# Performance work log

Hardware: AMD Instinct MI355X
Metric: run time of the kernel (lower is better)

The kernel has to match this reference:

```python
import jax, jax.numpy as jnp
import numpy as np

D = 256  # out_size / d_model
B, S = 8, 4096


def setup_inputs() -> dict:
    key = jax.random.key(0)
    ks = jax.random.split(key, 10)
    std = 1.0 / np.sqrt(D)
    x = jax.random.normal(ks[0], (B, S, D), dtype=jnp.float32)
    Wq = jax.random.uniform(ks[1], (D, D), jnp.float32, -std, std)
    bq = jax.random.uniform(ks[2], (D,), jnp.float32, -std, std)
    Wk = jax.random.uniform(ks[3], (D, D), jnp.float32, -std, std)
    bk = jax.random.uniform(ks[4], (D,), jnp.float32, -std, std)
    Wv = jax.random.uniform(ks[5], (D, D), jnp.float32, -std, std)
    bv = jax.random.uniform(ks[6], (D,), jnp.float32, -std, std)
    Wo = jax.random.uniform(ks[7], (D, D), jnp.float32, -std, std)
    bo = jax.random.uniform(ks[8], (D,), jnp.float32, -std, std)
    cv = jax.random.normal(ks[9], (D, 1), dtype=jnp.float32)
    return {"x": x, "Wq": Wq, "bq": bq, "Wk": Wk, "bk": bk,
            "Wv": Wv, "bv": bv, "Wo": Wo, "bo": bo, "cv": cv}


def reference(x, Wq, bq, Wk, bk, Wv, bv, Wo, bo, cv):
    # Local single-head attention: separate matmul / softmax / matmul
    q = jnp.einsum('bsd,de->bse', x, Wq) + bq
    k = jnp.einsum('bsd,de->bse', x, Wk) + bk
    v = jnp.einsum('bsd,de->bse', x, Wv) + bv
    scale = jnp.sqrt(jnp.asarray(D, dtype=x.dtype))
    scores = jnp.einsum('bqd,bkd->bqk', q, k) / scale  # [B,S,S]
    attn = jax.nn.softmax(scores, axis=-1)
    ctx = jnp.einsum('bqk,bkd->bqd', attn, v)
    logits = jnp.einsum('bsd,de->bse', ctx, Wo) + bo
    # Global context-vector pooling weights (softmax over sequence dim)
    w = jnp.einsum('bsd,dk->bsk', logits, cv)          # [B,S,1]
    nw = jax.nn.softmax(w, axis=1)
    return logits * nw
```

## Files before the change

### kernel.cpp

```cpp
#include <hip/hip_runtime.h>
#include <math.h>
#include <cstddef>
#include <cstdint>

#define B_ 8
#define S_ 4096
#define D_ 256

typedef __attribute__((ext_vector_type(8))) short short8v;
typedef __attribute__((ext_vector_type(4))) short short4v;
typedef __attribute__((ext_vector_type(4))) float float4v;

__device__ __forceinline__ unsigned short f2bf(float f) {
  unsigned u = __float_as_uint(f);
  return (unsigned short)((u + 0x7FFF + ((u >> 16) & 1)) >> 16);
}
__device__ __forceinline__ float bf2f(unsigned short h) {
  return __uint_as_float((unsigned)h << 16);
}
__device__ __forceinline__ unsigned packp(float p) {
  const unsigned short hh = f2bf(p);
  const unsigned short ll = f2bf(p - bf2f(hh));
  return ((unsigned)hh << 16) | (unsigned)ll;
}

__global__ __launch_bounds__(256) void wsplit_kernel(
    const float* __restrict__ Wq, const float* __restrict__ Wk,
    const float* __restrict__ Wv, const float* __restrict__ Wo,
    short* __restrict__ wsp) {
  const int mat = blockIdx.x >> 4;
  const int k0  = (blockIdx.x & 15) << 4;
  const float* W = (mat == 0) ? Wq : (mat == 1) ? Wk : (mat == 2) ? Wv : Wo;
  const int n = threadIdx.x;
  short8v h0, h1, l0, l1;
#pragma unroll
  for (int j = 0; j < 8; ++j) {
    float y = W[(size_t)(k0 + j) * 256 + n];
    unsigned short hh = f2bf(y);
    h0[j] = (short)hh; l0[j] = (short)f2bf(y - bf2f(hh));
    y = W[(size_t)(k0 + 8 + j) * 256 + n];
    hh = f2bf(y);
    h1[j] = (short)hh; l1[j] = (short)f2bf(y - bf2f(hh));
  }
  short* dh = wsp + (size_t)mat * 131072 + (size_t)n * 256 + k0;
  short* dl = dh + 65536;
  *(short8v*)(dh + 0) = h0; *(short8v*)(dh + 8) = h1;
  *(short8v*)(dl + 0) = l0; *(short8v*)(dl + 8) = l1;
}

__global__ __launch_bounds__(512, 2) void proj_qkv_mfma(
    const float* __restrict__ x, const short* __restrict__ wsp,
    const float* __restrict__ bq, const float* __restrict__ bk,
    const float* __restrict__ bvv,
    short* __restrict__ qh, short* __restrict__ ql,
    short* __restrict__ kh, short* __restrict__ kl,
    short* __restrict__ vth, short* __restrict__ vtl) {
  __shared__ __align__(16) short sWh[256 * 40];
  __shared__ __align__(16) short sWl[256 * 40];

  const int t    = threadIdx.x;
  const int w    = t >> 6;
  const int lane = t & 63;
  const int m    = lane & 15;
  const int quad = lane >> 4;
  const size_t r0 = (size_t)blockIdx.x * 128;
  const size_t srow = r0 + 16 * w + m;

  short8v xh[8], xl[8];
#pragma unroll
  for (int kk = 0; kk < 8; ++kk) {
    const float* xp = x + srow * 256 + kk * 32 + quad * 8;
    const float4 a = *(const float4*)xp;
    const float4 b2 = *(const float4*)(xp + 4);
    const float v[8] = {a.x, a.y, a.z, a.w, b2.x, b2.y, b2.z, b2.w};
    short8v h, l;
#pragma unroll
    for (int e = 0; e < 8; ++e) {
      const unsigned short hh = f2bf(v[e]);
      h[e] = (short)hh; l[e] = (short)f2bf(v[e] - bf2f(hh));
    }
    xh[kk] = h; xl[kk] = l;
  }

  const int nr   = t >> 1;
  const int kh16 = (t & 1) << 4;
  short8v rh0, rh1, rl0, rl1;
  {
    const short* gh = wsp + (size_t)nr * 256 + kh16;
    const short* gl = gh + 65536;
    rh0 = *(const short8v*)gh;       rh1 = *(const short8v*)(gh + 8);
    rl0 = *(const short8v*)gl;       rl1 = *(const short8v*)(gl + 8);
  }

#pragma unroll
  for (int p = 0; p < 3; ++p) {
    float4v acc[16];
#pragma unroll
    for (int nt = 0; nt < 16; ++nt) acc[nt] = (float4v){0.f, 0.f, 0.f, 0.f};

    for (int kk = 0; kk < 8; ++kk) {
      asm volatile("s_waitcnt lgkmcnt(0)" ::: "memory");
      __builtin_amdgcn_s_barrier();
      asm volatile("" ::: "memory");
      *(short8v*)&sWh[nr * 40 + kh16]     = rh0;
      *(short8v*)&sWh[nr * 40 + kh16 + 8] = rh1;
      *(short8v*)&sWl[nr * 40 + kh16]     = rl0;
      *(short8v*)&sWl[nr * 40 + kh16 + 8] = rl1;
      {
        const int np = (kk < 7) ? p : p + 1;
        const int nk = (kk < 7) ? kk + 1 : 0;
        if (np < 3) {
          const short* gh = wsp + (size_t)np * 131072 +
                            (size_t)nr * 256 + nk * 32 + kh16;
          const short* gl = gh + 65536;
          rh0 = *(const short8v*)gh;   rh1 = *(const short8v*)(gh + 8);
          rl0 = *(const short8v*)gl;   rl1 = *(const short8v*)(gl + 8);
        }
      }
      asm volatile("s_waitcnt lgkmcnt(0)" ::: "memory");
      __builtin_amdgcn_s_barrier();
      asm volatile("" ::: "memory");

      __builtin_amdgcn_s_setprio(1);
#pragma unroll
      for (int nt = 0; nt < 16; ++nt) {
        const short8v wh = *(const short8v*)&sWh[(nt * 16 + m) * 40 + quad * 8];
        const short8v wl = *(const short8v*)&sWl[(nt * 16 + m) * 40 + quad * 8];
        if (p < 2) {
          acc[nt] = __builtin_amdgcn_mfma_f32_16x16x32_bf16(wh, xh[kk], acc[nt], 0, 0, 0);
          acc[nt] = __builtin_amdgcn_mfma_f32_16x16x32_bf16(wh, xl[kk], acc[nt], 0, 0, 0);
          acc[nt] = __builtin_amdgcn_mfma_f32_16x16x32_bf16(wl, xh[kk], acc[nt], 0, 0, 0);
        } else {
          acc[nt] = __builtin_amdgcn_mfma_f32_16x16x32_bf16(xh[kk], wh, acc[nt], 0, 0, 0);
          acc[nt] = __builtin_amdgcn_mfma_f32_16x16x32_bf16(xh[kk], wl, acc[nt], 0, 0, 0);
          acc[nt] = __builtin_amdgcn_mfma_f32_16x16x32_bf16(xl[kk], wh, acc[nt], 0, 0, 0);
        }
      }
      __builtin_amdgcn_s_setprio(0);
    }

    if (p < 2) {
      const float scale = (p == 0) ? 0.0625f : 1.0f;
      short* oh = (p == 0) ? qh : kh;
      short* ol = (p == 0) ? ql : kl;
      const float* bias = (p == 0) ? bq : bk;
#pragma unroll
      for (int nt = 0; nt < 16; ++nt) {
        const float4 bb = *(const float4*)(bias + nt * 16 + quad * 4);
        const float bb4[4] = {bb.x, bb.y, bb.z, bb.w};
        short4v h4, l4;
#pragma unroll
        for (int r = 0; r < 4; ++r) {
          const float y = (acc[nt][r] + bb4[r]) * scale;
          const unsigned short hh = f2bf(y);
          h4[r] = (short)hh; l4[r] = (short)f2bf(y - bf2f(hh));
        }
        *(short4v*)(oh + srow * 256 + nt * 16 + quad * 4) = h4;
        *(short4v*)(ol + srow * 256 + nt * 16 + quad * 4) = l4;
      }
    } else {
      const int bidx = (int)(r0 >> 12);
      const size_t bD = (size_t)bidx * (D_ * (size_t)S_);
      const int sl0 = (int)(r0 & 4095) + 16 * w + quad * 4;
#pragma unroll
      for (int nt = 0; nt < 16; ++nt) {
        const int d = nt * 16 + m;
        const float bn = bvv[d];
        short4v h4, l4;
#pragma unroll
        for (int r = 0; r < 4; ++r) {
          const float y = acc[nt][r] + bn;
          const unsigned short hh = f2bf(y);
          h4[r] = (short)hh; l4[r] = (short)f2bf(y - bf2f(hh));
        }
        *(short4v*)(vth + bD + (size_t)d * S_ + sl0) = h4;
        *(short4v*)(vtl + bD + (size_t)d * S_ + sl0) = l4;
      }
    }
  }
}

__global__ __launch_bounds__(512, 2) void gemm_out_mfma(
    const float* __restrict__ ctx, const short* __restrict__ wsp,
    const float* __restrict__ bo, const float* __restrict__ cv,
    float* __restrict__ out, float* __restrict__ wvec) {
  __shared__ __align__(16) short sWh[256 * 40];
  __shared__ __align__(16) short sWl[256 * 40];

  const int t    = threadIdx.x;
  const int w    = t >> 6;
  const int lane = t & 63;
  const int m    = lane & 15;
  const int quad = lane >> 4;
  const size_t r0 = (size_t)blockIdx.x * 128;
  const size_t srow = r0 + 16 * w + m;
  const short* wbase = wsp + (size_t)3 * 131072;

  short8v ah[8], al[8];
#pragma unroll
  for (int kk = 0; kk < 8; ++kk) {
    const float* xp = ctx + srow * 256 + kk * 32 + quad * 8;
    const float4 a = *(const float4*)xp;
    const float4 b2 = *(const float4*)(xp + 4);
    const float v[8] = {a.x, a.y, a.z, a.w, b2.x, b2.y, b2.z, b2.w};
    short8v h, l;
#pragma unroll
    for (int e = 0; e < 8; ++e) {
      const unsigned short hh = f2bf(v[e]);
      h[e] = (short)hh; l[e] = (short)f2bf(v[e] - bf2f(hh));
    }
    ah[kk] = h; al[kk] = l;
  }

  const int nr   = t >> 1;
  const int kh16 = (t & 1) << 4;
  short8v rh0, rh1, rl0, rl1;
  {
    const short* gh = wbase + (size_t)nr * 256 + kh16;
    const short* gl = gh + 65536;
    rh0 = *(const short8v*)gh;       rh1 = *(const short8v*)(gh + 8);
    rl0 = *(const short8v*)gl;       rl1 = *(const short8v*)(gl + 8);
  }

  float4v acc[16];
#pragma unroll
  for (int nt = 0; nt < 16; ++nt) acc[nt] = (float4v){0.f, 0.f, 0.f, 0.f};

  for (int kk = 0; kk < 8; ++kk) {
    asm volatile("s_waitcnt lgkmcnt(0)" ::: "memory");
    __builtin_amdgcn_s_barrier();
    asm volatile("" ::: "memory");
    *(short8v*)&sWh[nr * 40 + kh16]     = rh0;
    *(short8v*)&sWh[nr * 40 + kh16 + 8] = rh1;
    *(short8v*)&sWl[nr * 40 + kh16]     = rl0;
    *(short8v*)&sWl[nr * 40 + kh16 + 8] = rl1;
    if (kk < 7) {
      const short* gh = wbase + (size_t)nr * 256 + (kk + 1) * 32 + kh16;
      const short* gl = gh + 65536;
      rh0 = *(const short8v*)gh;   rh1 = *(const short8v*)(gh + 8);
      rl0 = *(const short8v*)gl;   rl1 = *(const short8v*)(gl + 8);
    }
    asm volatile("s_waitcnt lgkmcnt(0)" ::: "memory");
    __builtin_amdgcn_s_barrier();
    asm volatile("" ::: "memory");

    __builtin_amdgcn_s_setprio(1);
#pragma unroll
    for (int nt = 0; nt < 16; ++nt) {
      const short8v wh = *(const short8v*)&sWh[(nt * 16 + m) * 40 + quad * 8];
      const short8v wl = *(const short8v*)&sWl[(nt * 16 + m) * 40 + quad * 8];
      acc[nt] = __builtin_amdgcn_mfma_f32_16x16x32_bf16(wh, ah[kk], acc[nt], 0, 0, 0);
      acc[nt] = __builtin_amdgcn_mfma_f32_16x16x32_bf16(wh, al[kk], acc[nt], 0, 0, 0);
      acc[nt] = __builtin_amdgcn_mfma_f32_16x16x32_bf16(wl, ah[kk], acc[nt], 0, 0, 0);
    }
    __builtin_amdgcn_s_setprio(0);
  }

  float wp = 0.f;
  float* orow = out + srow * 256;
#pragma unroll
  for (int nt = 0; nt < 16; ++nt) {
    const float4 bb = *(const float4*)(bo + nt * 16 + quad * 4);
    const float4 cc = *(const float4*)(cv + nt * 16 + quad * 4);
    float4 o;
    o.x = acc[nt][0] + bb.x; o.y = acc[nt][1] + bb.y;
    o.z = acc[nt][2] + bb.z; o.w = acc[nt][3] + bb.w;
    wp += o.x * cc.x + o.y * cc.y + o.z * cc.z + o.w * cc.w;
    *(float4*)(orow + nt * 16 + quad * 4) = o;
  }
  wp += __shfl_xor(wp, 16, 64);
  wp += __shfl_xor(wp, 32, 64);
  if (quad == 0) wvec[srow] = wp;
}

__global__ __launch_bounds__(512, 2) void flash_attn_mfma(
    const short* __restrict__ qh, const short* __restrict__ ql,
    const short* __restrict__ kh, const short* __restrict__ kl,
    const short* __restrict__ vth, const short* __restrict__ vtl,
    float* __restrict__ ctx) {
  __shared__ __align__(16) short sK[16896];
  __shared__ __align__(16) short sV[2][20480];
  __shared__ __align__(16) unsigned int sP[2][8][16][36];

  const int t    = threadIdx.x;
  const int w    = t >> 6;
  const int lane = t & 63;
  const int m    = lane & 15;
  const int quad = lane >> 4;
  const int q0   = blockIdx.x * 128;
  const int b    = blockIdx.y;
  const size_t sd = (size_t)b * (S_ * (size_t)D_);
  const size_t bD = (size_t)b * (D_ * (size_t)S_);

  short8v aqh[8], aql[8];
  {
    const size_t row = sd + (size_t)(q0 + 16 * w + m) * D_;
#pragma unroll
    for (int kk = 0; kk < 8; ++kk) {
      const size_t off = row + kk * 32 + quad * 8;
      aqh[kk] = *(const short8v*)(qh + off);
      aql[kk] = *(const short8v*)(ql + off);
    }
  }

  short8v ones;
#pragma unroll
  for (int e = 0; e < 8; ++e) ones[e] = (short)0x3F80;

  float4v acc[16];
#pragma unroll
  for (int dt = 0; dt < 16; ++dt) acc[dt] = (float4v){0.f, 0.f, 0.f, 0.f};
  float4v accl = (float4v){0.f, 0.f, 0.f, 0.f};
  float m_i = -INFINITY;

  const int kr0 = t >> 5;
  const int kc0 = (t & 31) << 3;
  const int vd  = t >> 1;
  const int vjh = (t & 1) << 4;

  short8v rKh0, rKh1, rKl0, rKl1;
  short8v rVh0, rVh1, rVl0, rVl1;

  {
    const size_t g0 = sd + (size_t)kr0 * D_ + kc0;
    const size_t g1 = sd + (size_t)(16 + kr0) * D_ + kc0;
    rKh0 = *(const short8v*)(kh + g0);
    rKh1 = *(const short8v*)(kh + g1);
    rKl0 = *(const short8v*)(kl + g0);
    rKl1 = *(const short8v*)(kl + g1);
  }

  for (int jt = 0; jt < 128; ++jt) {
    const int j0  = jt << 5;
    const int cur = jt & 1;
    const int old = cur ^ 1;

    *(short8v*)&sK[kr0 * 264 + kc0]               = rKh0;
    *(short8v*)&sK[(16 + kr0) * 264 + kc0]        = rKh1;
    *(short8v*)&sK[8448 + kr0 * 264 + kc0]        = rKl0;
    *(short8v*)&sK[8448 + (16 + kr0) * 264 + kc0] = rKl1;
    {
      const size_t g = bD + (size_t)vd * S_ + j0 + vjh;
      rVh0 = *(const short8v*)(vth + g);
      rVh1 = *(const short8v*)(vth + g + 8);
      rVl0 = *(const short8v*)(vtl + g);
      rVl1 = *(const short8v*)(vtl + g + 8);
    }
    asm volatile("s_waitcnt lgkmcnt(0)" ::: "memory");
    __builtin_amdgcn_s_barrier();
    asm volatile("" ::: "memory");

    float4v s0 = (float4v){0.f, 0.f, 0.f, 0.f};
    float4v s1 = (float4v){0.f, 0.f, 0.f, 0.f};
    __builtin_amdgcn_s_setprio(1);
#pragma unroll
    for (int kk = 0; kk < 8; ++kk) {
      const int co = kk * 32 + quad * 8;
      const short8v bh0 = *(const short8v*)&sK[m * 264 + co];
      const short8v bl0 = *(const short8v*)&sK[8448 + m * 264 + co];
      const short8v bh1 = *(const short8v*)&sK[(16 + m) * 264 + co];
      const short8v bl1 = *(const short8v*)&sK[8448 + (16 + m) * 264 + co];
      s0 = __builtin_amdgcn_mfma_f32_16x16x32_bf16(bh0, aqh[kk], s0, 0, 0, 0);
      s0 = __builtin_amdgcn_mfma_f32_16x16x32_bf16(bh0, aql[kk], s0, 0, 0, 0);
      s0 = __builtin_amdgcn_mfma_f32_16x16x32_bf16(bl0, aqh[kk], s0, 0, 0, 0);
      s1 = __builtin_amdgcn_mfma_f32_16x16x32_bf16(bh1, aqh[kk], s1, 0, 0, 0);
      s1 = __builtin_amdgcn_mfma_f32_16x16x32_bf16(bh1, aql[kk], s1, 0, 0, 0);
      s1 = __builtin_amdgcn_mfma_f32_16x16x32_bf16(bl1, aqh[kk], s1, 0, 0, 0);
    }
    __builtin_amdgcn_s_setprio(0);

    float alpha_p = 1.0f;
    bool fired = false;
    {
      float mx = fmaxf(fmaxf(fmaxf(s0[0], s0[1]), fmaxf(s0[2], s0[3])),
                       fmaxf(fmaxf(s1[0], s1[1]), fmaxf(s1[2], s1[3])));
      mx = fmaxf(mx, __shfl_xor(mx, 16, 64));
      mx = fmaxf(mx, __shfl_xor(mx, 32, 64));
      if (__any(mx > m_i + 8.0f)) {
        const float mnew = fmaxf(m_i, mx);
        alpha_p = __expf(m_i - mnew);
        m_i = mnew;
        fired = true;
      }
    }

    {
      uint4 w0, w1;
      w0.x = packp(__expf(s0[0] - m_i));
      w0.y = packp(__expf(s0[1] - m_i));
      w0.z = packp(__expf(s0[2] - m_i));
      w0.w = packp(__expf(s0[3] - m_i));
      w1.x = packp(__expf(s1[0] - m_i));
      w1.y = packp(__expf(s1[1] - m_i));
      w1.z = packp(__expf(s1[2] - m_i));
      w1.w = packp(__expf(s1[3] - m_i));
      *(uint4*)&sP[cur][w][m][4 * quad]      = w0;
      *(uint4*)&sP[cur][w][m][16 + 4 * quad] = w1;
    }

    if (jt > 0) {
      short8v ph, pl;
      {
        const uint4 pa = *(const uint4*)&sP[old][w][m][quad * 8];
        const uint4 pb = *(const uint4*)&sP[old][w][m][quad * 8 + 4];
        ph[0] = (short)(pa.x >> 16); pl[0] = (short)(pa.x & 0xffff);
        ph[1] = (short)(pa.y >> 16); pl[1] = (short)(pa.y & 0xffff);
        ph[2] = (short)(pa.z >> 16); pl[2] = (short)(pa.z & 0xffff);
        ph[3] = (short)(pa.w >> 16); pl[3] = (short)(pa.w & 0xffff);
        ph[4] = (short)(pb.x >> 16); pl[4] = (short)(pb.x & 0xffff);
        ph[5] = (short)(pb.y >> 16); pl[5] = (short)(pb.y & 0xffff);
        ph[6] = (short)(pb.z >> 16); pl[6] = (short)(pb.z & 0xffff);
        ph[7] = (short)(pb.w >> 16); pl[7] = (short)(pb.w & 0xffff);
      }
      const short* sVo = &sV[old][0];
      __builtin_amdgcn_s_setprio(1);
      accl = __builtin_amdgcn_mfma_f32_16x16x32_bf16(ph, ones, accl, 0, 0, 0);
      accl = __builtin_amdgcn_mfma_f32_16x16x32_bf16(pl, ones, accl, 0, 0, 0);
#pragma unroll
      for (int dt = 0; dt < 16; ++dt) {
        const int vr = (dt * 16 + m) * 40 + quad * 8;
        const short8v bh = *(const short8v*)&sVo[vr];
        const short8v bl = *(const short8v*)&sVo[10240 + vr];
        acc[dt] = __builtin_amdgcn_mfma_f32_16x16x32_bf16(ph, bh, acc[dt], 0, 0, 0);
        acc[dt] = __builtin_amdgcn_mfma_f32_16x16x32_bf16(ph, bl, acc[dt], 0, 0, 0);
        acc[dt] = __builtin_amdgcn_mfma_f32_16x16x32_bf16(pl, bh, acc[dt], 0, 0, 0);
      }
      __builtin_amdgcn_s_setprio(0);
    }

    if (fired) {
      float al[4];
#pragma unroll
      for (int r = 0; r < 4; ++r) al[r] = __shfl(alpha_p, 20 * quad + r, 64);
#pragma unroll
      for (int dt = 0; dt < 16; ++dt)
#pragma unroll
        for (int r = 0; r < 4; ++r) acc[dt][r] *= al[r];
#pragma unroll
      for (int r = 0; r < 4; ++r) accl[r] *= al[r];
    }

    {
      short* sVc = &sV[cur][0];
      *(short8v*)&sVc[vd * 40 + vjh]             = rVh0;
      *(short8v*)&sVc[vd * 40 + vjh + 8]         = rVh1;
      *(short8v*)&sVc[10240 + vd * 40 + vjh]     = rVl0;
      *(short8v*)&sVc[10240 + vd * 40 + vjh + 8] = rVl1;
    }
    if (jt < 127) {
      const int j0n = j0 + 32;
      const size_t g0 = sd + (size_t)(j0n + kr0) * D_ + kc0;
      const size_t g1 = sd + (size_t)(j0n + 16 + kr0) * D_ + kc0;
      rKh0 = *(const short8v*)(kh + g0);
      rKh1 = *(const short8v*)(kh + g1);
      rKl0 = *(const short8v*)(kl + g0);
      rKl1 = *(const short8v*)(kl + g1);
    }
    asm volatile("s_waitcnt lgkmcnt(0)" ::: "memory");
    __builtin_amdgcn_s_barrier();
    asm volatile("" ::: "memory");
  }

  {
    short8v ph, pl;
    {
      const uint4 pa = *(const uint4*)&sP[1][w][m][quad * 8];
      const uint4 pb = *(const uint4*)&sP[1][w][m][quad * 8 + 4];
      ph[0] = (short)(pa.x >> 16); pl[0] = (short)(pa.x & 0xffff);
      ph[1] = (short)(pa.y >> 16); pl[1] = (short)(pa.y & 0xffff);
      ph[2] = (short)(pa.z >> 16); pl[2] = (short)(pa.z & 0xffff);
      ph[3] = (short)(pa.w >> 16); pl[3] = (short)(pa.w & 0xffff);
      ph[4] = (short)(pb.x >> 16); pl[4] = (short)(pb.x & 0xffff);
      ph[5] = (short)(pb.y >> 16); pl[5] = (short)(pb.y & 0xffff);
      ph[6] = (short)(pb.z >> 16); pl[6] = (short)(pb.z & 0xffff);
      ph[7] = (short)(pb.w >> 16); pl[7] = (short)(pb.w & 0xffff);
    }
    const short* sVo = &sV[1][0];
    accl = __builtin_amdgcn_mfma_f32_16x16x32_bf16(ph, ones, accl, 0, 0, 0);
    accl = __builtin_amdgcn_mfma_f32_16x16x32_bf16(pl, ones, accl, 0, 0, 0);
#pragma unroll
    for (int dt = 0; dt < 16; ++dt) {
      const int vr = (dt * 16 + m) * 40 + quad * 8;
      const short8v bh = *(const short8v*)&sVo[vr];
      const short8v bl = *(const short8v*)&sVo[10240 + vr];
      acc[dt] = __builtin_amdgcn_mfma_f32_16x16x32_bf16(ph, bh, acc[dt], 0, 0, 0);
      acc[dt] = __builtin_amdgcn_mfma_f32_16x16x32_bf16(ph, bl, acc[dt], 0, 0, 0);
      acc[dt] = __builtin_amdgcn_mfma_f32_16x16x32_bf16(pl, bh, acc[dt], 0, 0, 0);
    }
  }

#pragma unroll
  for (int r = 0; r < 4; ++r) {
    const float inv = 1.0f / accl[r];
    float* cp = ctx + sd + (size_t)(q0 + 16 * w + quad * 4 + r) * D_ + m;
#pragma unroll
    for (int dt = 0; dt < 16; ++dt) cp[dt * 16] = acc[dt][r] * inv;
  }
}

__global__ __launch_bounds__(256) void softmax_scale_kernel(
    float* __restrict__ out, const float* __restrict__ wv) {
  __shared__ float red[4];
  const int t = threadIdx.x;
  const int wave = t >> 6, lane = t & 63;
  const int b = blockIdx.x >> 8;
  const float* wb = wv + (size_t)b * S_;

  float mx = -INFINITY;
#pragma unroll
  for (int i = 0; i < 16; ++i) mx = fmaxf(mx, wb[t + (i << 8)]);
#pragma unroll
  for (int off = 32; off > 0; off >>= 1) mx = fmaxf(mx, __shfl_xor(mx, off, 64));
  if (lane == 0) red[wave] = mx;
  __syncthreads();
  const float M = fmaxf(fmaxf(red[0], red[1]), fmaxf(red[2], red[3]));
  float sum = 0.f;
#pragma unroll
  for (int i = 0; i < 16; ++i) sum += __expf(wb[t + (i << 8)] - M);
#pragma unroll
  for (int off = 32; off > 0; off >>= 1) sum += __shfl_xor(sum, off, 64);
  __syncthreads();
  if (lane == 0) red[wave] = sum;
  __syncthreads();
  const float inv = 1.0f / (red[0] + red[1] + red[2] + red[3]);

  float4* o4 = (float4*)out;
  const size_t g0 = (size_t)blockIdx.x * 1024 + t;
#pragma unroll
  for (int i = 0; i < 4; ++i) {
    const size_t g = g0 + (size_t)(i << 8);
    const float sc = __expf(wv[g >> 6] - M) * inv;
    float4 vv = o4[g];
    vv.x *= sc; vv.y *= sc; vv.z *= sc; vv.w *= sc;
    o4[g] = vv;
  }
}

extern "C" void kernel_launch(void* const* d_in, const int* in_sizes, int n_in,
                              void* d_out, int out_size, void* d_ws, size_t ws_size,
                              hipStream_t stream) {
  const float* x  = (const float*)d_in[0];
  const float* Wq = (const float*)d_in[1];
  const float* bq = (const float*)d_in[2];
  const float* Wk = (const float*)d_in[3];
  const float* bk = (const float*)d_in[4];
  const float* Wv = (const float*)d_in[5];
  const float* bv = (const float*)d_in[6];
  const float* Wo = (const float*)d_in[7];
  const float* bo = (const float*)d_in[8];
  const float* cv = (const float*)d_in[9];
  float* out = (float*)d_out;

  const size_t N = (size_t)B_ * S_ * D_;
  short* qh  = (short*)d_ws;
  short* ql  = qh + N;
  short* kh  = ql + N;
  short* kl  = kh + N;
  short* vth = kl + N;
  short* vtl = vth + N;
  float* ctx = (float*)(vtl + N);
  float* w   = ctx + N;
  short* wsp = (short*)(w + (size_t)B_ * S_);

  wsplit_kernel<<<64, 256, 0, stream>>>(Wq, Wk, Wv, Wo, wsp);
  proj_qkv_mfma<<<256, 512, 0, stream>>>(x, wsp, bq, bk, bv,
                                         qh, ql, kh, kl, vth, vtl);
  flash_attn_mfma<<<dim3(32, 8), 512, 0, stream>>>(qh, ql, kh, kl, vth, vtl, ctx);
  gemm_out_mfma<<<256, 512, 0, stream>>>(ctx, wsp, bo, cv, out, w);
  softmax_scale_kernel<<<2048, 256, 0, stream>>>(out, w);
}
```

Before: 598.5 us.

## Split PV matmul across waves by output column tiles, single-buffer sV/sP

```diff
diff --git a/kernel.cpp b/kernel.cpp
--- a/kernel.cpp
+++ b/kernel.cpp
@@ -279,8 +279,11 @@
     const short* __restrict__ vth, const short* __restrict__ vtl,
     float* __restrict__ ctx) {
   __shared__ __align__(16) short sK[16896];
-  __shared__ __align__(16) short sV[2][20480];
-  __shared__ __align__(16) unsigned int sP[2][8][16][36];
+  __shared__ __align__(16) short sV[20480];
+  __shared__ __align__(16) unsigned int sP[8][16][36];
+  __shared__ __align__(16) float sAlpha[8][16];
+  __shared__ __align__(16) int sF[8];
+  __shared__ __align__(16) float sL[128];
 
   const int t    = threadIdx.x;
   const int w    = t >> 6;
@@ -307,9 +310,12 @@
 #pragma unroll
   for (int e = 0; e < 8; ++e) ones[e] = (short)0x3F80;
 
-  float4v acc[16];
-#pragma unroll
-  for (int dt = 0; dt < 16; ++dt) acc[dt] = (float4v){0.f, 0.f, 0.f, 0.f};
+  float4v acc[8][2];
+#pragma unroll
+  for (int qt = 0; qt < 8; ++qt) {
+    acc[qt][0] = (float4v){0.f, 0.f, 0.f, 0.f};
+    acc[qt][1] = (float4v){0.f, 0.f, 0.f, 0.f};
+  }
   float4v accl = (float4v){0.f, 0.f, 0.f, 0.f};
   float m_i = -INFINITY;
 
@@ -331,9 +337,7 @@
   }
 
   for (int jt = 0; jt < 128; ++jt) {
-    const int j0  = jt << 5;
-    const int cur = jt & 1;
-    const int old = cur ^ 1;
+    const int j0 = jt << 5;
 
     *(short8v*)&sK[kr0 * 264 + kc0]               = rKh0;
     *(short8v*)&sK[(16 + kr0) * 264 + kc0]        = rKh1;
@@ -370,7 +374,7 @@
     __builtin_amdgcn_s_setprio(0);
 
     float alpha_p = 1.0f;
-    bool fired = false;
+    int fired = 0;
     {
       float mx = fmaxf(fmaxf(fmaxf(s0[0], s0[1]), fmaxf(s0[2], s0[3])),
                        fmaxf(fmaxf(s1[0], s1[1]), fmaxf(s1[2], s1[3])));
@@ -380,9 +384,16 @@
         const float mnew = fmaxf(m_i, mx);
         alpha_p = __expf(m_i - mnew);
         m_i = mnew;
-        fired = true;
-      }
-    }
+        fired = 1;
+        float al[4];
+#pragma unroll
+        for (int r = 0; r < 4; ++r) al[r] = __shfl(alpha_p, 20 * quad + r, 64);
+#pragma unroll
+        for (int r = 0; r < 4; ++r) accl[r] *= al[r];
+      }
+    }
+    if (quad == 0) sAlpha[w][m] = alpha_p;
+    if (lane == 0) sF[w] = fired;
 
     {
       uint4 w0, w1;
@@ -394,59 +405,14 @@
       w1.y = packp(__expf(s1[1] - m_i));
       w1.z = packp(__expf(s1[2] - m_i));
       w1.w = packp(__expf(s1[3] - m_i));
-      *(uint4*)&sP[cur][w][m][4 * quad]      = w0;
-      *(uint4*)&sP[cur][w][m][16 + 4 * quad] = w1;
-    }
-
-    if (jt > 0) {
-      short8v ph, pl;
-      {
-        const uint4 pa = *(const uint4*)&sP[old][w][m][quad * 8];
-        const uint4 pb = *(const uint4*)&sP[old][w][m][quad * 8 + 4];
-        ph[0] = (short)(pa.x >> 16); pl[0] = (short)(pa.x & 0xffff);
-        ph[1] = (short)(pa.y >> 16); pl[1] = (short)(pa.y & 0xffff);
-        ph[2] = (short)(pa.z >> 16); pl[2] = (short)(pa.z & 0xffff);
-        ph[3] = (short)(pa.w >> 16); pl[3] = (short)(pa.w & 0xffff);
-        ph[4] = (short)(pb.x >> 16); pl[4] = (short)(pb.x & 0xffff);
-        ph[5] = (short)(pb.y >> 16); pl[5] = (short)(pb.y & 0xffff);
-        ph[6] = (short)(pb.z >> 16); pl[6] = (short)(pb.z & 0xffff);
-        ph[7] = (short)(pb.w >> 16); pl[7] = (short)(pb.w & 0xffff);
-      }
-      const short* sVo = &sV[old][0];
-      __builtin_amdgcn_s_setprio(1);
-      accl = __builtin_amdgcn_mfma_f32_16x16x32_bf16(ph, ones, accl, 0, 0, 0);
-      accl = __builtin_amdgcn_mfma_f32_16x16x32_bf16(pl, ones, accl, 0, 0, 0);
-#pragma unroll
-      for (int dt = 0; dt < 16; ++dt) {
-        const int vr = (dt * 16 + m) * 40 + quad * 8;
-        const short8v bh = *(const short8v*)&sVo[vr];
-        const short8v bl = *(const short8v*)&sVo[10240 + vr];
-        acc[dt] = __builtin_amdgcn_mfma_f32_16x16x32_bf16(ph, bh, acc[dt], 0, 0, 0);
-        acc[dt] = __builtin_amdgcn_mfma_f32_16x16x32_bf16(ph, bl, acc[dt], 0, 0, 0);
-        acc[dt] = __builtin_amdgcn_mfma_f32_16x16x32_bf16(pl, bh, acc[dt], 0, 0, 0);
-      }
-      __builtin_amdgcn_s_setprio(0);
-    }
-
-    if (fired) {
-      float al[4];
-#pragma unroll
-      for (int r = 0; r < 4; ++r) al[r] = __shfl(alpha_p, 20 * quad + r, 64);
-#pragma unroll
-      for (int dt = 0; dt < 16; ++dt)
-#pragma unroll
-        for (int r = 0; r < 4; ++r) acc[dt][r] *= al[r];
-#pragma unroll
-      for (int r = 0; r < 4; ++r) accl[r] *= al[r];
-    }
-
-    {
-      short* sVc = &sV[cur][0];
-      *(short8v*)&sVc[vd * 40 + vjh]             = rVh0;
-      *(short8v*)&sVc[vd * 40 + vjh + 8]         = rVh1;
-      *(short8v*)&sVc[10240 + vd * 40 + vjh]     = rVl0;
-      *(short8v*)&sVc[10240 + vd * 40 + vjh + 8] = rVl1;
-    }
+      *(uint4*)&sP[w][m][4 * quad]      = w0;
+      *(uint4*)&sP[w][m][16 + 4 * quad] = w1;
+    }
+
+    *(short8v*)&sV[vd * 40 + vjh]               = rVh0;
+    *(short8v*)&sV[vd * 40 + vjh + 8]           = rVh1;
+    *(short8v*)&sV[10240 + vd * 40 + vjh]       = rVl0;
+    *(short8v*)&sV[10240 + vd * 40 + vjh + 8]   = rVl1;
     if (jt < 127) {
       const int j0n = j0 + 32;
       const size_t g0 = sd + (size_t)(j0n + kr0) * D_ + kc0;
@@ -459,42 +425,79 @@
     asm volatile("s_waitcnt lgkmcnt(0)" ::: "memory");
     __builtin_amdgcn_s_barrier();
     asm volatile("" ::: "memory");
-  }
-
-  {
-    short8v ph, pl;
+
     {
-      const uint4 pa = *(const uint4*)&sP[1][w][m][quad * 8];
-      const uint4 pb = *(const uint4*)&sP[1][w][m][quad * 8 + 4];
-      ph[0] = (short)(pa.x >> 16); pl[0] = (short)(pa.x & 0xffff);
-      ph[1] = (short)(pa.y >> 16); pl[1] = (short)(pa.y & 0xffff);
-      ph[2] = (short)(pa.z >> 16); pl[2] = (short)(pa.z & 0xffff);
-      ph[3] = (short)(pa.w >> 16); pl[3] = (short)(pa.w & 0xffff);
-      ph[4] = (short)(pb.x >> 16); pl[4] = (short)(pb.x & 0xffff);
-      ph[5] = (short)(pb.y >> 16); pl[5] = (short)(pb.y & 0xffff);
-      ph[6] = (short)(pb.z >> 16); pl[6] = (short)(pb.z & 0xffff);
-      ph[7] = (short)(pb.w >> 16); pl[7] = (short)(pb.w & 0xffff);
-    }
-    const short* sVo = &sV[1][0];
-    accl = __builtin_amdgcn_mfma_f32_16x16x32_bf16(ph, ones, accl, 0, 0, 0);
-    accl = __builtin_amdgcn_mfma_f32_16x16x32_bf16(pl, ones, accl, 0, 0, 0);
-#pragma unroll
-    for (int dt = 0; dt < 16; ++dt) {
-      const int vr = (dt * 16 + m) * 40 + quad * 8;
-      const short8v bh = *(const short8v*)&sVo[vr];
-      const short8v bl = *(const short8v*)&sVo[10240 + vr];
-      acc[dt] = __builtin_amdgcn_mfma_f32_16x16x32_bf16(ph, bh, acc[dt], 0, 0, 0);
-      acc[dt] = __builtin_amdgcn_mfma_f32_16x16x32_bf16(ph, bl, acc[dt], 0, 0, 0);
-      acc[dt] = __builtin_amdgcn_mfma_f32_16x16x32_bf16(pl, bh, acc[dt], 0, 0, 0);
-    }
-  }
-
-#pragma unroll
-  for (int r = 0; r < 4; ++r) {
-    const float inv = 1.0f / accl[r];
-    float* cp = ctx + sd + (size_t)(q0 + 16 * w + quad * 4 + r) * D_ + m;
-#pragma unroll
-    for (int dt = 0; dt < 16; ++dt) cp[dt * 16] = acc[dt][r] * inv;
+      const uint4 f0 = *(const uint4*)&sF[0];
+      const uint4 f1 = *(const uint4*)&sF[4];
+      if (f0.x | f0.y | f0.z | f0.w | f1.x | f1.y | f1.z | f1.w) {
+#pragma unroll
+        for (int qt = 0; qt < 8; ++qt) {
+          const float4 alf = *(const float4*)&sAlpha[qt][quad << 2];
+          const float a4[4] = {alf.x, alf.y, alf.z, alf.w};
+#pragma unroll
+          for (int r = 0; r < 4; ++r) {
+            acc[qt][0][r] *= a4[r];
+            acc[qt][1][r] *= a4[r];
+          }
+        }
+      }
+    }
+
+    __builtin_amdgcn_s_setprio(1);
+    {
+      const int vr0 = ((w << 1) * 16 + m) * 40 + quad * 8;
+      const short8v bh0 = *(const short8v*)&sV[vr0];
+      const short8v bl0 = *(const short8v*)&sV[10240 + vr0];
+      const short8v bh1 = *(const short8v*)&sV[vr0 + 640];
+      const short8v bl1 = *(const short8v*)&sV[10240 + vr0 + 640];
+#pragma unroll
+      for (int qt = 0; qt < 8; ++qt) {
+        short8v ph, pl;
+        {
+          const uint4 pa = *(const uint4*)&sP[qt][m][quad * 8];
+          const uint4 pb = *(const uint4*)&sP[qt][m][quad * 8 + 4];
+          ph[0] = (short)(pa.x >> 16); pl[0] = (short)(pa.x & 0xffff);
+          ph[1] = (short)(pa.y >> 16); pl[1] = (short)(pa.y & 0xffff);
+          ph[2] = (short)(pa.z >> 16); pl[2] = (short)(pa.z & 0xffff);
+          ph[3] = (short)(pa.w >> 16); pl[3] = (short)(pa.w & 0xffff);
+          ph[4] = (short)(pb.x >> 16); pl[4] = (short)(pb.x & 0xffff);
+          ph[5] = (short)(pb.y >> 16); pl[5] = (short)(pb.y & 0xffff);
+          ph[6] = (short)(pb.z >> 16); pl[6] = (short)(pb.z & 0xffff);
+          ph[7] = (short)(pb.w >> 16); pl[7] = (short)(pb.w & 0xffff);
+        }
+        if (qt == w) {
+          accl = __builtin_amdgcn_mfma_f32_16x16x32_bf16(ph, ones, accl, 0, 0, 0);
+          accl = __builtin_amdgcn_mfma_f32_16x16x32_bf16(pl, ones, accl, 0, 0, 0);
+        }
+        acc[qt][0] = __builtin_amdgcn_mfma_f32_16x16x32_bf16(ph, bh0, acc[qt][0], 0, 0, 0);
+        acc[qt][0] = __builtin_amdgcn_mfma_f32_16x16x32_bf16(ph, bl0, acc[qt][0], 0, 0, 0);
+        acc[qt][0] = __builtin_amdgcn_mfma_f32_16x16x32_bf16(pl, bh0, acc[qt][0], 0, 0, 0);
+        acc[qt][1] = __builtin_amdgcn_mfma_f32_16x16x32_bf16(ph, bh1, acc[qt][1], 0, 0, 0);
+        acc[qt][1] = __builtin_amdgcn_mfma_f32_16x16x32_bf16(ph, bl1, acc[qt][1], 0, 0, 0);
+        acc[qt][1] = __builtin_amdgcn_mfma_f32_16x16x32_bf16(pl, bh1, acc[qt][1], 0, 0, 0);
+      }
+    }
+    __builtin_amdgcn_s_setprio(0);
+  }
+
+  if (m == 0) {
+#pragma unroll
+    for (int r = 0; r < 4; ++r) sL[16 * w + 4 * quad + r] = accl[r];
+  }
+  __syncthreads();
+#pragma unroll
+  for (int qt = 0; qt < 8; ++qt) {
+    const float4 lf = *(const float4*)&sL[16 * qt + (quad << 2)];
+    const float inv4[4] = {1.0f / lf.x, 1.0f / lf.y, 1.0f / lf.z, 1.0f / lf.w};
+#pragma unroll
+    for (int dtl = 0; dtl < 2; ++dtl) {
+      const int d = ((w << 1) + dtl) * 16 + m;
+#pragma unroll
+      for (int r = 0; r < 4; ++r) {
+        ctx[sd + (size_t)(q0 + 16 * qt + 4 * quad + r) * D_ + d] =
+            acc[qt][dtl][r] * inv4[r];
+      }
+    }
   }
 }
 
```

Result: faster. 578.3 us (-3.4%).
